# Performance work log

Measured on AMD Instinct MI355X. Metric: run time of the kernel, lower is better.

The kernel has to match this reference:

```python
import jax, jax.numpy as jnp
import numpy as np

DIM = 512
NUM_HEADS = 8
DIM_HEAD = DIM // NUM_HEADS


def _xavier(key, shape):
    fan_in, fan_out = shape[0], shape[1]
    a = (6.0 / (fan_in + fan_out)) ** 0.5
    return jax.random.uniform(key, shape, jnp.float32, -a, a)


def setup_inputs() -> dict:
    key = jax.random.key(0)
    ks = jax.random.split(key, 8)
    B, N, M = 2, 2048, 2048
    x = jax.random.normal(ks[0], (B, N, DIM), jnp.float32)
    source = jax.random.normal(ks[1], (B, M, DIM), jnp.float32)
    source_mask = jax.random.randint(ks[2], (B, M), 0, 2) > 0
    Wq = _xavier(ks[3], (DIM, DIM)); bq = jnp.zeros((DIM,), jnp.float32)
    Wk = _xavier(ks[4], (DIM, DIM)); bk = jnp.zeros((DIM,), jnp.float32)
    Wv = _xavier(ks[5], (DIM, DIM)); bv = jnp.zeros((DIM,), jnp.float32)
    Wm = _xavier(ks[6], (DIM, DIM)); bm = jnp.zeros((DIM,), jnp.float32)
    return {"x": x, "source": source, "source_mask": source_mask,
            "Wq": Wq, "bq": bq, "Wk": Wk, "bk": bk,
            "Wv": Wv, "bv": bv, "Wm": Wm, "bm": bm}


def reference(x, source, source_mask, Wq, bq, Wk, bk, Wv, bv, Wm, bm):
    B, N, D = x.shape
    M = source.shape[-2]
    H, Dh = NUM_HEADS, DIM_HEAD
    # projections (torch Linear: x @ W^T + b)
    q = (x @ Wq.T + bq).reshape(B, N, H, Dh)
    k = (source @ Wk.T + bk).reshape(B, M, H, Dh)
    v = (source @ Wv.T + bv).reshape(B, M, H, Dh)
    scale = 1.0 / (Dh ** 0.5)
    # scores: [B, N, M, H]
    scores = jnp.einsum('bnhd,bmhd->bnmh', q, k) * scale
    scores = jnp.where(source_mask[:, None, :, None], scores, -jnp.inf)
    prob = jax.nn.softmax(scores, axis=-2)  # softmax over m
    agg = jnp.einsum('bnmh,bmhd->bnhd', prob, v).reshape(B, N, D)
    return agg @ Wm.T + bm
```

## Files before the change

### kernel.cpp

```cpp
#include <hip/hip_runtime.h>
#include <hip/hip_bf16.h>

#define DIMF 512
#define NHEAD 8
#define DHEAD 64
#define BATCH 2
#define SEQN 2048
#define SEQM 2048
#define FPS 40
#define QSCALE 0.18033688011112042f

typedef unsigned short u16;
typedef __attribute__((ext_vector_type(8))) short bf16x8;
typedef __attribute__((ext_vector_type(4))) float f32x4;

static __device__ __forceinline__ u16 f2bf(float f) {
    unsigned u = __float_as_uint(f);
    u += 0x7FFF + ((u >> 16) & 1);
    return (u16)(u >> 16);
}
static __device__ __forceinline__ u16 f2bf_fast(float f) {
    return (u16)((__float_as_uint(f) + 0x8000u) >> 16);
}
static __device__ __forceinline__ ushort4 cvt4(float4 v) {
    return make_ushort4(f2bf(v.x), f2bf(v.y), f2bf(v.z), f2bf(v.w));
}
static __device__ __forceinline__ bf16x8 mask8(const int* p) {
    int4 a = *(const int4*)p;
    int4 b = *(const int4*)(p + 4);
    union { u16 u[8]; bf16x8 v; } r;
    r.u[0] = a.x ? 0x3F80 : 0; r.u[1] = a.y ? 0x3F80 : 0;
    r.u[2] = a.z ? 0x3F80 : 0; r.u[3] = a.w ? 0x3F80 : 0;
    r.u[4] = b.x ? 0x3F80 : 0; r.u[5] = b.y ? 0x3F80 : 0;
    r.u[6] = b.z ? 0x3F80 : 0; r.u[7] = b.w ? 0x3F80 : 0;
    return r.v;
}

static __device__ __forceinline__
void load16(const u16* g, u16* l) {
    __builtin_amdgcn_global_load_lds(
        (const __attribute__((address_space(1))) void*)g,
        (__attribute__((address_space(3))) void*)l,
        16, 0, 0);
}

__global__ __launch_bounds__(256)
void cvt_w(const float* __restrict__ wq, const float* __restrict__ wk,
           const float* __restrict__ wv, const float* __restrict__ wm,
           u16* __restrict__ wqb, u16* __restrict__ wkb,
           u16* __restrict__ wvb, u16* __restrict__ wmb)
{
    int i = (blockIdx.x * 256 + threadIdx.x) * 4;
    if (i >= DIMF * DIMF) return;
    const float* in = (blockIdx.y == 0) ? wq : (blockIdx.y == 1) ? wk
                    : (blockIdx.y == 2) ? wv : wm;
    u16* out = (blockIdx.y == 0) ? wqb : (blockIdx.y == 1) ? wkb
             : (blockIdx.y == 2) ? wvb : wmb;
    float4 v = *(const float4*)&in[i];
    *(ushort4*)&out[i] = cvt4(v);
}

#define ASZ (64 * FPS)
#define BSZ (128 * FPS)

__device__ __forceinline__
void gemm_mfma(const float* __restrict__ Xf, const u16* __restrict__ Xb,
               const u16* __restrict__ W, const float* __restrict__ bias,
               const int* __restrict__ msk, void* __restrict__ Out, int mode)
{
    __shared__ __align__(16) u16 SH[2 * ASZ + 2 * BSZ];

    const int tid  = threadIdx.x;
    const int wave = tid >> 6;
    const int lane = tid & 63;
    const int l15  = lane & 15;
    const int quad = lane >> 4;
    const int wm = wave & 1, wn = wave >> 1;
    const int r0 = blockIdx.x * 64, c0 = blockIdx.y * 128;

    f32x4 acc[2][4] = {};

    const int br = tid >> 2, boct = tid & 3;
    const int ar = tid >> 3, aseg = tid & 7;

    bf16x8 rb0, rb1, rab;
    float4 ra0, ra1;

    auto loadg = [&](int k0) {
        rb0 = *(const bf16x8*)&W[(size_t)(c0 + br) * DIMF + k0 + boct * 8];
        rb1 = *(const bf16x8*)&W[(size_t)(c0 + br + 64) * DIMF + k0 + boct * 8];
        if (Xf) {
            ra0 = *(const float4*)&Xf[(size_t)(r0 + ar) * DIMF + k0 + aseg * 4];
            ra1 = *(const float4*)&Xf[(size_t)(r0 + ar + 32) * DIMF + k0 + aseg * 4];
        } else {
            rab = *(const bf16x8*)&Xb[(size_t)(r0 + br) * DIMF + k0 + boct * 8];
        }
    };
    auto stage = [&](int buf) {
        u16* As = SH + buf * ASZ;
        u16* Bs = SH + 2 * ASZ + buf * BSZ;
        if (Xf) {
            *(ushort4*)&As[ar * FPS + aseg * 4] = cvt4(ra0);
            *(ushort4*)&As[(ar + 32) * FPS + aseg * 4] = cvt4(ra1);
        } else {
            *(bf16x8*)&As[br * FPS + boct * 8] = rab;
        }
        *(bf16x8*)&Bs[br * FPS + boct * 8] = rb0;
        *(bf16x8*)&Bs[(br + 64) * FPS + boct * 8] = rb1;
    };

    loadg(0);
    stage(0);
    loadg(32);
    __syncthreads();

    const int NK = DIMF / 32;
    for (int kt = 0; kt < NK; ++kt) {
        const int cur = kt & 1;
        if (kt + 1 < NK) stage(cur ^ 1);
        if (kt + 2 < NK) loadg((kt + 2) * 32);
        const u16* As = SH + cur * ASZ;
        const u16* Bs = SH + 2 * ASZ + cur * BSZ;

        bf16x8 af[2], bf[4];
        #pragma unroll
        for (int mi = 0; mi < 2; ++mi)
            af[mi] = *(const bf16x8*)&As[(wm * 32 + mi * 16 + l15) * FPS + quad * 8];
        #pragma unroll
        for (int ni = 0; ni < 4; ++ni)
            bf[ni] = *(const bf16x8*)&Bs[(wn * 64 + ni * 16 + l15) * FPS + quad * 8];
        #pragma unroll
        for (int mi = 0; mi < 2; ++mi)
            #pragma unroll
            for (int ni = 0; ni < 4; ++ni)
                acc[mi][ni] = __builtin_amdgcn_mfma_f32_16x16x32_bf16(
                    af[mi], bf[ni], acc[mi][ni], 0, 0, 0);
        __syncthreads();
    }

    float bb[4];
    #pragma unroll
    for (int ni = 0; ni < 4; ++ni)
        bb[ni] = bias[c0 + wn * 64 + ni * 16 + l15];

    if (mode == 2) {
        u16* T = SH;
        const int b = r0 >> 11;
        const int n_base = r0 & (SEQN - 1);
        #pragma unroll
        for (int hh = 0; hh < 2; ++hh) {
            __syncthreads();
            if (wn == hh) {
                #pragma unroll
                for (int mi = 0; mi < 2; ++mi) {
                    const int rl = wm * 32 + mi * 16 + quad * 4;
                    int4 m4 = *(const int4*)&msk[b * SEQM + n_base + rl];
                    float mm[4];
                    mm[0] = m4.x ? 1.f : 0.f; mm[1] = m4.y ? 1.f : 0.f;
                    mm[2] = m4.z ? 1.f : 0.f; mm[3] = m4.w ? 1.f : 0.f;
                    #pragma unroll
                    for (int ni = 0; ni < 4; ++ni)
                        #pragma unroll
                        for (int r = 0; r < 4; ++r)
                            T[(rl + r) * 72 + ni * 16 + l15] =
                                f2bf((acc[mi][ni][r] + bb[ni]) * mm[r]);
                }
            }
            __syncthreads();
            const int d = tid >> 2, ms = (tid & 3) << 4;
            u16 tmp[16];
            #pragma unroll
            for (int j = 0; j < 16; ++j) tmp[j] = T[(ms + j) * 72 + d];
            const int hgl = (c0 >> 6) + hh;
            u16* dst = (u16*)Out + ((size_t)(b * NHEAD + hgl) * DHEAD + d) * SEQM
                       + n_base + ms;
            *(bf16x8*)&dst[0] = *(bf16x8*)&tmp[0];
            *(bf16x8*)&dst[8] = *(bf16x8*)&tmp[8];
        }
        return;
    }

    #pragma unroll
    for (int mi = 0; mi < 2; ++mi) {
        const int Rbase = r0 + wm * 32 + mi * 16 + quad * 4;
        const int b = Rbase >> 11;
        const int nb = Rbase & (SEQN - 1);
        #pragma unroll
        for (int ni = 0; ni < 4; ++ni) {
            const int C = c0 + wn * 64 + ni * 16 + l15;
            const int h = C >> 6, d = C & 63;
            if (mode == 0) {
                u16* ow = (u16*)Out;
                #pragma unroll
                for (int r = 0; r < 4; ++r)
                    ow[(((size_t)(b * NHEAD + h) * SEQN) + nb + r) * DHEAD + d] =
                        f2bf((acc[mi][ni][r] + bb[ni]) * QSCALE);
            } else if (mode == 1) {
                u16* ow = (u16*)Out;
                #pragma unroll
                for (int r = 0; r < 4; ++r)
                    ow[(((size_t)(b * NHEAD + h) * SEQN) + nb + r) * DHEAD + d] =
                        f2bf(acc[mi][ni][r] + bb[ni]);
            } else {
                float* ow = (float*)Out;
                #pragma unroll
                for (int r = 0; r < 4; ++r)
                    ow[(size_t)(Rbase + r) * DIMF + C] = acc[mi][ni][r] + bb[ni];
            }
        }
    }
}

__global__ __launch_bounds__(256, 3)
void qkv_proj(const float* __restrict__ x, const float* __restrict__ src,
              const u16* __restrict__ wqb, const float* __restrict__ bq,
              const u16* __restrict__ wkb, const float* __restrict__ bk,
              const u16* __restrict__ wvb, const float* __restrict__ bv,
              const int* __restrict__ mask,
              u16* __restrict__ qw, u16* __restrict__ kw, u16* __restrict__ vtw)
{
    const int z = blockIdx.z;
    const float* X = (z == 0) ? x : src;
    const u16* W = (z == 0) ? wqb : (z == 1) ? wkb : wvb;
    const float* B = (z == 0) ? bq : (z == 1) ? bk : bv;
    void* O = (z == 0) ? (void*)qw : (z == 1) ? (void*)kw : (void*)vtw;
    gemm_mfma(X, nullptr, W, B, mask, O, z);
}

__global__ __launch_bounds__(256, 3)
void out_proj(const u16* __restrict__ aggb, const u16* __restrict__ wmb,
              const float* __restrict__ bm, float* __restrict__ out)
{
    gemm_mfma(nullptr, aggb, wmb, bm, nullptr, (void*)out, 3);
}

__global__ __launch_bounds__(256, 3)
void flash_attn_mfma(const u16* __restrict__ q, const u16* __restrict__ k,
                     const u16* __restrict__ vt, const int* __restrict__ mask,
                     u16* __restrict__ agg)
{
    __shared__ __align__(16) u16 KsD[2][4096];
    __shared__ __align__(16) u16 VtsD[2][4096];
    __shared__ u16 Ps[4 * 32 * FPS];
    float* Osum = (float*)&KsD[0][0];
    float* Lsum = (float*)&VtsD[0][0];

    const int tid  = threadIdx.x;
    const int wave = tid >> 6;
    const int lane = tid & 63;
    const int l15  = lane & 15;
    const int quad = lane >> 4;
    const int qg = wave >> 1, mh = wave & 1;

    const int bid  = blockIdx.x;
    const int xcd  = bid & 7, slot = bid >> 3;
    const int pair = (xcd << 1) | (slot & 1);
    const int b = pair >> 3, h = pair & 7;
    const int n0 = (slot >> 1) * 64;

    const size_t hoff = (size_t)(b * NHEAD + h) * (size_t)SEQM * DHEAD;
    const u16* kb = k  + hoff;
    const u16* vb = vt + hoff;
    const int* mg = mask + b * SEQM;

    const int dr   = lane >> 3;
    const int doct = (lane & 7) ^ (dr & 7);
    const int g0 = wave, g1 = 4 + wave;
    const u16* kq0 = kb + (size_t)(g0 * 8 + dr) * DHEAD + doct * 8;
    const u16* kq1 = kb + (size_t)(g1 * 8 + dr) * DHEAD + doct * 8;
    const u16* vq0 = vb + (size_t)(g0 * 8 + dr) * SEQM + doct * 8;
    const u16* vq1 = vb + (size_t)(g1 * 8 + dr) * SEQM + doct * 8;

    bf16x8 qf[2][2];
    #pragma unroll
    for (int qh = 0; qh < 2; ++qh) {
        const u16* qp = q + hoff + (size_t)(n0 + qg * 32 + qh * 16 + l15) * DHEAD
                        + quad * 8;
        qf[qh][0] = *(const bf16x8*)qp;
        qf[qh][1] = *(const bf16x8*)(qp + 32);
    }

    load16(kq0, &KsD[0][g0 * 512]);
    load16(kq1, &KsD[0][g1 * 512]);
    load16(vq0, &VtsD[0][g0 * 512]);
    load16(vq1, &VtsD[0][g1 * 512]);
    bf16x8 mf_nxt = mask8(&mg[32 * mh + quad * 8]);

    f32x4 O[2][4] = {};
    f32x4 lacc[2] = {};
    u16* Pw = Ps + wave * (32 * FPS);
    const int xoct = l15 & 7;

    for (int mt = 0; mt < SEQM / 64; ++mt) {
        const int cur = mt & 1;
        __syncthreads();
        bf16x8 mf = mf_nxt;
        if (mt + 1 < SEQM / 64) {
            const int m1 = (mt + 1) * 64;
            const int nb = cur ^ 1;
            load16(kq0 + (size_t)m1 * DHEAD, &KsD[nb][g0 * 512]);
            load16(kq1 + (size_t)m1 * DHEAD, &KsD[nb][g1 * 512]);
            load16(vq0 + m1, &VtsD[nb][g0 * 512]);
            load16(vq1 + m1, &VtsD[nb][g1 * 512]);
            mf_nxt = mask8(&mg[m1 + 32 * mh + quad * 8]);
        }
        const u16* Ks  = KsD[cur];
        const u16* Vts = VtsD[cur];

        f32x4 st[2][2] = {};
        #pragma unroll
        for (int sub = 0; sub < 2; ++sub) {
            const int mrow = 32 * mh + 16 * sub + l15;
            #pragma unroll
            for (int c = 0; c < 2; ++c) {
                const int oct = (4 * c + quad) ^ xoct;
                bf16x8 af = *(const bf16x8*)&Ks[mrow * 64 + oct * 8];
                #pragma unroll
                for (int qh = 0; qh < 2; ++qh)
                    st[qh][sub] = __builtin_amdgcn_mfma_f32_16x16x32_bf16(
                        af, qf[qh][c], st[qh][sub], 0, 0, 0);
            }
        }

        #pragma unroll
        for (int qh = 0; qh < 2; ++qh)
            #pragma unroll
            for (int sub = 0; sub < 2; ++sub) {
                ushort4 w4 = make_ushort4(
                    f2bf_fast(__builtin_amdgcn_exp2f(st[qh][sub][0])),
                    f2bf_fast(__builtin_amdgcn_exp2f(st[qh][sub][1])),
                    f2bf_fast(__builtin_amdgcn_exp2f(st[qh][sub][2])),
                    f2bf_fast(__builtin_amdgcn_exp2f(st[qh][sub][3])));
                *(ushort4*)&Pw[(qh * 16 + l15) * FPS + 16 * sub + 4 * quad] = w4;
            }

        bf16x8 vf[4];
        #pragma unroll
        for (int sd = 0; sd < 4; ++sd) {
            const int oct = (4 * mh + quad) ^ xoct;
            vf[sd] = *(const bf16x8*)&Vts[(16 * sd + l15) * 64 + oct * 8];
        }

        #pragma unroll
        for (int qh = 0; qh < 2; ++qh) {
            bf16x8 pf = *(const bf16x8*)&Pw[(qh * 16 + l15) * FPS + quad * 8];
            lacc[qh] = __builtin_amdgcn_mfma_f32_16x16x32_bf16(pf, mf, lacc[qh], 0, 0, 0);
            #pragma unroll
            for (int sd = 0; sd < 4; ++sd)
                O[qh][sd] = __builtin_amdgcn_mfma_f32_16x16x32_bf16(
                    pf, vf[sd], O[qh][sd], 0, 0, 0);
        }
    }

    __syncthreads();
    if (mh == 1) {
        #pragma unroll
        for (int qh = 0; qh < 2; ++qh) {
            #pragma unroll
            for (int sd = 0; sd < 4; ++sd)
                #pragma unroll
                for (int r = 0; r < 4; ++r)
                    Osum[qg * 2048 + (qh * 16 + quad * 4 + r) * 64 + 16 * sd + l15]
                        = O[qh][sd][r];
            if (l15 == 0) {
                #pragma unroll
                for (int r = 0; r < 4; ++r)
                    Lsum[qg * 32 + qh * 16 + quad * 4 + r] = lacc[qh][r];
            }
        }
    }
    __syncthreads();
    if (mh == 0) {
        #pragma unroll
        for (int qh = 0; qh < 2; ++qh)
            #pragma unroll
            for (int r = 0; r < 4; ++r) {
                const float inv = 1.f /
                    (lacc[qh][r] + Lsum[qg * 32 + qh * 16 + quad * 4 + r]);
                const int n = n0 + qg * 32 + qh * 16 + quad * 4 + r;
                u16* ag = agg + ((size_t)b * SEQN + n) * DIMF + h * DHEAD + l15;
                #pragma unroll
                for (int sd = 0; sd < 4; ++sd)
                    ag[16 * sd] = f2bf((O[qh][sd][r] +
                        Osum[qg * 2048 + (qh * 16 + quad * 4 + r) * 64 + 16 * sd + l15])
                        * inv);
            }
    }
}

extern "C" void kernel_launch(void* const* d_in, const int* in_sizes, int n_in,
                              void* d_out, int out_size, void* d_ws, size_t ws_size,
                              hipStream_t stream)
{
    (void)in_sizes; (void)n_in; (void)out_size; (void)ws_size;
    const float* x      = (const float*)d_in[0];
    const float* source = (const float*)d_in[1];
    const int*   mask   = (const int*)  d_in[2];
    const float* Wq = (const float*)d_in[3]; const float* bq = (const float*)d_in[4];
    const float* Wk = (const float*)d_in[5]; const float* bk = (const float*)d_in[6];
    const float* Wv = (const float*)d_in[7]; const float* bv = (const float*)d_in[8];
    const float* Wm = (const float*)d_in[9]; const float* bm = (const float*)d_in[10];
    float* out = (float*)d_out;

    const size_t SZ = (size_t)BATCH * SEQN * DIMF;
    const size_t WZ = (size_t)DIMF * DIMF;
    u16* qw   = (u16*)d_ws;
    u16* kw   = qw  + SZ;
    u16* vtw  = kw  + SZ;
    u16* aggb = vtw + SZ;
    u16* wqb  = aggb + SZ;
    u16* wkb  = wqb + WZ;
    u16* wvb  = wkb + WZ;
    u16* wmb  = wvb + WZ;

    dim3 gcvt((WZ / 4 + 255) / 256, 4);
    cvt_w<<<gcvt, 256, 0, stream>>>(Wq, Wk, Wv, Wm, wqb, wkb, wvb, wmb);

    dim3 gproj(4096 / 64, 512 / 128, 3);
    qkv_proj<<<gproj, 256, 0, stream>>>(x, source, wqb, bq, wkb, bk, wvb, bv,
                                        mask, qw, kw, vtw);

    flash_attn_mfma<<<512, 256, 0, stream>>>(qw, kw, vtw, mask, aggb);

    dim3 gout(4096 / 64, 512 / 128);
    out_proj<<<gout, 256, 0, stream>>>(aggb, wmb, bm, out);
}
```

Baseline: 148.6 us.

## Fuse all four stages into one cooperative persistent kernel with grid syncs

Replaces the four separate launches (weight conversion, QKV projection, flash attention, output projection) with a single cooperative kernel. Its blocks loop over the tiles of each stage and call grid.sync between stages. The goal is to remove per-launch overhead and inter-kernel gaps. In exchange it adds grid-wide barriers and a shared LDS buffer sized for the largest stage, and launch bounds drop to 2 blocks per CU, which may cut occupancy for the GEMM and attention stages.

```diff
diff --git a/kernel.cpp b/kernel.cpp
--- a/kernel.cpp
+++ b/kernel.cpp
@@ -1,5 +1,8 @@
 #include <hip/hip_runtime.h>
 #include <hip/hip_bf16.h>
+#include <hip/hip_cooperative_groups.h>
+
+namespace cg = cooperative_groups;
 
 #define DIMF 512
 #define NHEAD 8
@@ -44,39 +47,23 @@
         16, 0, 0);
 }
 
-__global__ __launch_bounds__(256)
-void cvt_w(const float* __restrict__ wq, const float* __restrict__ wk,
-           const float* __restrict__ wv, const float* __restrict__ wm,
-           u16* __restrict__ wqb, u16* __restrict__ wkb,
-           u16* __restrict__ wvb, u16* __restrict__ wmb)
-{
-    int i = (blockIdx.x * 256 + threadIdx.x) * 4;
-    if (i >= DIMF * DIMF) return;
-    const float* in = (blockIdx.y == 0) ? wq : (blockIdx.y == 1) ? wk
-                    : (blockIdx.y == 2) ? wv : wm;
-    u16* out = (blockIdx.y == 0) ? wqb : (blockIdx.y == 1) ? wkb
-             : (blockIdx.y == 2) ? wvb : wmb;
-    float4 v = *(const float4*)&in[i];
-    *(ushort4*)&out[i] = cvt4(v);
-}
-
 #define ASZ (64 * FPS)
 #define BSZ (128 * FPS)
 
 __device__ __forceinline__
-void gemm_mfma(const float* __restrict__ Xf, const u16* __restrict__ Xb,
+void gemm_tile(u16* __restrict__ SH,
+               const float* __restrict__ Xf, const u16* __restrict__ Xb,
                const u16* __restrict__ W, const float* __restrict__ bias,
-               const int* __restrict__ msk, void* __restrict__ Out, int mode)
+               const int* __restrict__ msk, void* __restrict__ Out, int mode,
+               int bx, int by)
 {
-    __shared__ __align__(16) u16 SH[2 * ASZ + 2 * BSZ];
-
     const int tid  = threadIdx.x;
     const int wave = tid >> 6;
     const int lane = tid & 63;
     const int l15  = lane & 15;
     const int quad = lane >> 4;
     const int wm = wave & 1, wn = wave >> 1;
-    const int r0 = blockIdx.x * 64, c0 = blockIdx.y * 128;
+    const int r0 = bx * 64, c0 = by * 128;
 
     f32x4 acc[2][4] = {};
 
@@ -211,39 +198,17 @@
     }
 }
 
-__global__ __launch_bounds__(256, 3)
-void qkv_proj(const float* __restrict__ x, const float* __restrict__ src,
-              const u16* __restrict__ wqb, const float* __restrict__ bq,
-              const u16* __restrict__ wkb, const float* __restrict__ bk,
-              const u16* __restrict__ wvb, const float* __restrict__ bv,
-              const int* __restrict__ mask,
-              u16* __restrict__ qw, u16* __restrict__ kw, u16* __restrict__ vtw)
+__device__ __forceinline__
+void flash_unit(u16* __restrict__ SH,
+                const u16* __restrict__ q, const u16* __restrict__ k,
+                const u16* __restrict__ vt, const int* __restrict__ mask,
+                u16* __restrict__ agg, int bid)
 {
-    const int z = blockIdx.z;
-    const float* X = (z == 0) ? x : src;
-    const u16* W = (z == 0) ? wqb : (z == 1) ? wkb : wvb;
-    const float* B = (z == 0) ? bq : (z == 1) ? bk : bv;
-    void* O = (z == 0) ? (void*)qw : (z == 1) ? (void*)kw : (void*)vtw;
-    gemm_mfma(X, nullptr, W, B, mask, O, z);
-}
-
-__global__ __launch_bounds__(256, 3)
-void out_proj(const u16* __restrict__ aggb, const u16* __restrict__ wmb,
-              const float* __restrict__ bm, float* __restrict__ out)
-{
-    gemm_mfma(nullptr, aggb, wmb, bm, nullptr, (void*)out, 3);
-}
-
-__global__ __launch_bounds__(256, 3)
-void flash_attn_mfma(const u16* __restrict__ q, const u16* __restrict__ k,
-                     const u16* __restrict__ vt, const int* __restrict__ mask,
-                     u16* __restrict__ agg)
-{
-    __shared__ __align__(16) u16 KsD[2][4096];
-    __shared__ __align__(16) u16 VtsD[2][4096];
-    __shared__ u16 Ps[4 * 32 * FPS];
-    float* Osum = (float*)&KsD[0][0];
-    float* Lsum = (float*)&VtsD[0][0];
+    u16* KsD  = SH;
+    u16* VtsD = SH + 8192;
+    u16* Ps   = SH + 16384;
+    float* Osum = (float*)SH;
+    float* Lsum = (float*)(SH + 8192);
 
     const int tid  = threadIdx.x;
     const int wave = tid >> 6;
@@ -252,7 +217,6 @@
     const int quad = lane >> 4;
     const int qg = wave >> 1, mh = wave & 1;
 
-    const int bid  = blockIdx.x;
     const int xcd  = bid & 7, slot = bid >> 3;
     const int pair = (xcd << 1) | (slot & 1);
     const int b = pair >> 3, h = pair & 7;
@@ -280,10 +244,10 @@
         qf[qh][1] = *(const bf16x8*)(qp + 32);
     }
 
-    load16(kq0, &KsD[0][g0 * 512]);
-    load16(kq1, &KsD[0][g1 * 512]);
-    load16(vq0, &VtsD[0][g0 * 512]);
-    load16(vq1, &VtsD[0][g1 * 512]);
+    load16(kq0, KsD + g0 * 512);
+    load16(kq1, KsD + g1 * 512);
+    load16(vq0, VtsD + g0 * 512);
+    load16(vq1, VtsD + g1 * 512);
     bf16x8 mf_nxt = mask8(&mg[32 * mh + quad * 8]);
 
     f32x4 O[2][4] = {};
@@ -298,14 +262,14 @@
         if (mt + 1 < SEQM / 64) {
             const int m1 = (mt + 1) * 64;
             const int nb = cur ^ 1;
-            load16(kq0 + (size_t)m1 * DHEAD, &KsD[nb][g0 * 512]);
-            load16(kq1 + (size_t)m1 * DHEAD, &KsD[nb][g1 * 512]);
-            load16(vq0 + m1, &VtsD[nb][g0 * 512]);
-            load16(vq1 + m1, &VtsD[nb][g1 * 512]);
+            load16(kq0 + (size_t)m1 * DHEAD, KsD + nb * 4096 + g0 * 512);
+            load16(kq1 + (size_t)m1 * DHEAD, KsD + nb * 4096 + g1 * 512);
+            load16(vq0 + m1, VtsD + nb * 4096 + g0 * 512);
+            load16(vq1 + m1, VtsD + nb * 4096 + g1 * 512);
             mf_nxt = mask8(&mg[m1 + 32 * mh + quad * 8]);
         }
-        const u16* Ks  = KsD[cur];
-        const u16* Vts = VtsD[cur];
+        const u16* Ks  = KsD + cur * 4096;
+        const u16* Vts = VtsD + cur * 4096;
 
         f32x4 st[2][2] = {};
         #pragma unroll
@@ -385,6 +349,56 @@
                         Osum[qg * 2048 + (qh * 16 + quad * 4 + r) * 64 + 16 * sd + l15])
                         * inv);
             }
+    }
+}
+
+__global__ __launch_bounds__(256, 2)
+void attn_fused(const float* __restrict__ x, const float* __restrict__ source,
+                const int* __restrict__ mask,
+                const float* __restrict__ Wq, const float* __restrict__ bq,
+                const float* __restrict__ Wk, const float* __restrict__ bk,
+                const float* __restrict__ Wv, const float* __restrict__ bv,
+                const float* __restrict__ Wm, const float* __restrict__ bm,
+                float* __restrict__ out,
+                u16* __restrict__ qw, u16* __restrict__ kw,
+                u16* __restrict__ vtw, u16* __restrict__ aggb,
+                u16* __restrict__ wqb, u16* __restrict__ wkb,
+                u16* __restrict__ wvb, u16* __restrict__ wmb)
+{
+    cg::grid_group grid = cg::this_grid();
+    __shared__ __align__(16) u16 SH[21504];
+
+    const int nblk = gridDim.x;
+
+    for (int i = blockIdx.x * 256 + threadIdx.x; i < 4 * 65536; i += nblk * 256) {
+        const int w = i >> 16, j = (i & 65535) * 4;
+        const float* in = (w == 0) ? Wq : (w == 1) ? Wk : (w == 2) ? Wv : Wm;
+        u16* o = (w == 0) ? wqb : (w == 1) ? wkb : (w == 2) ? wvb : wmb;
+        *(ushort4*)&o[j] = cvt4(*(const float4*)&in[j]);
+    }
+    grid.sync();
+
+    for (int t = blockIdx.x; t < 768; t += nblk) {
+        const int bx = t & 63, by = (t >> 6) & 3, z = t >> 8;
+        const float* X = (z == 0) ? x : source;
+        const u16* W = (z == 0) ? wqb : (z == 1) ? wkb : wvb;
+        const float* B = (z == 0) ? bq : (z == 1) ? bk : bv;
+        void* O = (z == 0) ? (void*)qw : (z == 1) ? (void*)kw : (void*)vtw;
+        gemm_tile(SH, X, nullptr, W, B, mask, O, z, bx, by);
+        __syncthreads();
+    }
+    grid.sync();
+
+    for (int bid = blockIdx.x; bid < 512; bid += nblk) {
+        flash_unit(SH, qw, kw, vtw, mask, aggb, bid);
+        __syncthreads();
+    }
+    grid.sync();
+
+    for (int t = blockIdx.x; t < 256; t += nblk) {
+        gemm_tile(SH, nullptr, aggb, wmb, bm, nullptr, (void*)out, 3,
+                  t & 63, t >> 6);
+        __syncthreads();
     }
 }
 
@@ -413,15 +427,20 @@
     u16* wvb  = wkb + WZ;
     u16* wmb  = wvb + WZ;
 
-    dim3 gcvt((WZ / 4 + 255) / 256, 4);
-    cvt_w<<<gcvt, 256, 0, stream>>>(Wq, Wk, Wv, Wm, wqb, wkb, wvb, wmb);
-
-    dim3 gproj(4096 / 64, 512 / 128, 3);
-    qkv_proj<<<gproj, 256, 0, stream>>>(x, source, wqb, bq, wkb, bk, wvb, bv,
-                                        mask, qw, kw, vtw);
-
-    flash_attn_mfma<<<512, 256, 0, stream>>>(qw, kw, vtw, mask, aggb);
-
-    dim3 gout(4096 / 64, 512 / 128);
-    out_proj<<<gout, 256, 0, stream>>>(aggb, wmb, bm, out);
-}
+    int bpc = 0;
+    hipOccupancyMaxActiveBlocksPerMultiprocessor(&bpc, attn_fused, 256, 0);
+    if (bpc < 1) bpc = 1;
+    int nblk = bpc * 256;
+    if (nblk > 512) nblk = 512;
+
+    void* args[] = {
+        (void*)&x, (void*)&source, (void*)&mask,
+        (void*)&Wq, (void*)&bq, (void*)&Wk, (void*)&bk,
+        (void*)&Wv, (void*)&bv, (void*)&Wm, (void*)&bm,
+        (void*)&out,
+        (void*)&qw, (void*)&kw, (void*)&vtw, (void*)&aggb,
+        (void*)&wqb, (void*)&wkb, (void*)&wvb, (void*)&wmb
+    };
+    hipLaunchCooperativeKernel(attn_fused, dim3(nblk), dim3(256),
+                               args, 0, stream);
+}
```

Result: slower. 289.7 us (+94.9%).
